# Optimization experiments

Hardware: AMD Instinct MI355X
Metric: run time of the kernel (lower is better)

The kernel has to match this reference:

```python
import jax, jax.numpy as jnp
import numpy as np

N = 3072          # n_vertices
D = 512           # embedding_size (hardcoded in module)
ALPHA = 0.2       # LeakyReLU slope
AVG_DEG = 32
NEG_INF = -9e15
N_ITERS = 10
TRIPLET_MARGIN = 400.0


def setup_inputs() -> dict:
    key = jax.random.key(0)
    ks = jax.random.split(key, 14)
    s = 0.05  # weight init scale
    emb = jax.random.normal(ks[0], (N, D), dtype=jnp.float32) * 0.1
    # symmetric 0/1 adjacency, no self loops, density ~ AVG_DEG/N
    u = jax.random.uniform(ks[1], (N, N))
    A = jnp.triu((u < (AVG_DEG / N)).astype(jnp.float32), 1)
    adj = A + A.T
    rn = lambda k, shp: jax.random.normal(k, shp, dtype=jnp.float32) * s
    return {
        "embeddings": emb,
        "adj": adj,
        "W_n": rn(ks[2], (D, D)), "a_src_n": rn(ks[3], (D,)), "a_dst_n": rn(ks[4], (D,)),
        "W_nn": rn(ks[5], (D, D)), "a_src_nn": rn(ks[6], (D,)), "a_dst_nn": rn(ks[7], (D,)),
        "W_u": rn(ks[8], (2 * D, D)), "b_u": jnp.zeros((D,), dtype=jnp.float32),
        "W_g": rn(ks[9], (D, D)), "a_src_g": rn(ks[10], (D,)), "a_dst_g": rn(ks[11], (D,)),
    }


def _gat_attention(h, adj, W, a_src, a_dst):
    # standard pyGAT layer: Wh = hW; e_ij = LeakyReLU(a_src.Wh_i + a_dst.Wh_j)
    Wh = h @ W                                   # [N, D]
    e = jax.nn.leaky_relu((Wh @ a_src)[:, None] + (Wh @ a_dst)[None, :], ALPHA)
    att = jax.nn.softmax(jnp.where(adj > 0, e, NEG_INF), axis=1)  # [N, N]
    return att, Wh


def reference(embeddings, adj, W_n, a_src_n, a_dst_n, W_nn, a_src_nn, a_dst_nn,
              W_u, b_u, W_g, a_src_g, a_dst_g):
    n = embeddings.shape[0]
    inv_adj = 1.0 - adj - jnp.eye(n, dtype=adj.dtype)  # non-neighbors, no self
    emb = embeddings
    for _ in range(N_ITERS):
        att_n, Wh_n = _gat_attention(emb, adj, W_n, a_src_n, a_dst_n)
        neigh = jax.nn.elu(att_n @ Wh_n)               # concat=True -> ELU
        att_nn, Wh_nn = _gat_attention(emb, inv_adj, W_nn, a_src_nn, a_dst_nn)
        non_neigh = jax.nn.elu(att_nn @ Wh_nn)
        cat = jnp.concatenate([neigh, non_neigh], axis=1)  # [N, 2D]
        emb = jax.nn.relu(emb + cat @ W_u + b_u)
    sq = jnp.sum(emb * emb, axis=1)
    d2 = sq[:, None] + sq[None, :] - 2.0 * (emb @ emb.T)
    dist = jnp.sqrt(jnp.maximum(d2, 1e-12))            # [N, N]
    embedding_loss = jnp.sum(dist * (-adj))
    triplet_loss = jnp.maximum(embedding_loss + TRIPLET_MARGIN, 0.0)
    # glimpse layer returns the attention matrix itself
    att_g, _ = _gat_attention(emb, adj, W_g, a_src_g, a_dst_g)
    confidence = jnp.max(att_g, axis=1)
    log_conf = jnp.mean(jnp.log(confidence + 1e-8) - jnp.log(1e-8))
    return jnp.stack([triplet_loss, embedding_loss, log_conf])
```

## Files before the change

### kernel.cpp

```cpp
#include <hip/hip_runtime.h>
#include <math.h>

#define N_V 3072
#define D_E 512
#define EDGE_CAP 128
constexpr float LRELU_ALPHA = 0.2f;
constexpr float NEG_INF_F = -9e15f;

typedef __attribute__((ext_vector_type(8))) short bf16x8;
typedef __attribute__((ext_vector_type(4))) float f32x4;
typedef __attribute__((ext_vector_type(4))) unsigned short ushort4v;
typedef __attribute__((ext_vector_type(2))) unsigned short ushort2v;

__device__ inline unsigned short f2bf(float f) {
    union { float f; unsigned int u; } x; x.f = f;
    unsigned int r = x.u + 0x7fffu + ((x.u >> 16) & 1u);
    return (unsigned short)(r >> 16);
}
__device__ inline float bf2f(unsigned short b) {
    union { unsigned int u; float f; } x; x.u = ((unsigned int)b) << 16;
    return x.f;
}

__device__ inline void xcd_swizzle(int& bx, int& by) {
    int gx = gridDim.x, nwg = gx * gridDim.y;
    int flat = by * gx + bx;
    int q = nwg >> 3;
    int swz = (flat & 7) * q + (flat >> 3);
    bx = swz % gx; by = swz / gx;
}

template<int EPI>
__global__ __launch_bounds__(256) void gemm_bf16(
    const unsigned short* __restrict__ A,
    const unsigned short* __restrict__ BT,
    int M, int N, int K,
    unsigned short* __restrict__ C0, int ldc0,
    unsigned short* __restrict__ C1,
    const float* __restrict__ addv,
    const float* __restrict__ bias,
    float* __restrict__ Cf)
{
    constexpr int BM = 128, BN = 64, BK = 64;
    __shared__ unsigned short As[BM * BK];
    __shared__ unsigned short Bs[BN * BK];
    const int tid  = threadIdx.x;
    int bxi = blockIdx.x, byi = blockIdx.y;
    xcd_swizzle(bxi, byi);
    const int bm   = byi * BM, bn = bxi * BN;
    const int lane = tid & 63, wid = tid >> 6;
    const int wr   = wid >> 1, wc = wid & 1;
    const int lr   = lane & 15, lk = lane >> 4;

    f32x4 acc[4][2];
    #pragma unroll
    for (int i = 0; i < 4; ++i)
        #pragma unroll
        for (int j = 0; j < 2; ++j)
            acc[i][j] = (f32x4)(0.f);

    auto asp = (__attribute__((address_space(3))) unsigned short*)As;
    auto bsp = (__attribute__((address_space(3))) unsigned short*)Bs;

    for (int k0 = 0; k0 < K; k0 += BK) {
        #pragma unroll
        for (int l = 0; l < 4; ++l) {
            int li = l * 256 + tid;
            int row = li >> 3, slot = li & 7;
            int gs = slot ^ (row & 7);
            __builtin_amdgcn_global_load_lds(
                (const __attribute__((address_space(1))) void*)(A + (size_t)(bm + row) * K + k0 + gs * 8),
                (__attribute__((address_space(3))) void*)(asp + li * 8), 16, 0, 0);
        }
        #pragma unroll
        for (int l = 0; l < 2; ++l) {
            int li = l * 256 + tid;
            int row = li >> 3, slot = li & 7;
            int gs = slot ^ (row & 7);
            __builtin_amdgcn_global_load_lds(
                (const __attribute__((address_space(1))) void*)(BT + (size_t)(bn + row) * K + k0 + gs * 8),
                (__attribute__((address_space(3))) void*)(bsp + li * 8), 16, 0, 0);
        }
        __syncthreads();

        #pragma unroll
        for (int ks = 0; ks < 2; ++ks) {
            bf16x8 af[4], bfr[2];
            #pragma unroll
            for (int fm = 0; fm < 4; ++fm) {
                int row = wr * 64 + fm * 16 + lr;
                int sl = (ks * 4 + lk) ^ (row & 7);
                af[fm] = *(const bf16x8*)(As + row * BK + sl * 8);
            }
            #pragma unroll
            for (int fn = 0; fn < 2; ++fn) {
                int col = wc * 32 + fn * 16 + lr;
                int sl = (ks * 4 + lk) ^ (col & 7);
                bfr[fn] = *(const bf16x8*)(Bs + col * BK + sl * 8);
            }
            #pragma unroll
            for (int fm = 0; fm < 4; ++fm)
                #pragma unroll
                for (int fn = 0; fn < 2; ++fn)
                    acc[fm][fn] = __builtin_amdgcn_mfma_f32_16x16x32_bf16(
                        af[fm], bfr[fn], acc[fm][fn], 0, 0, 0);
        }
        __syncthreads();
    }

    #pragma unroll
    for (int fm = 0; fm < 4; ++fm) {
        #pragma unroll
        for (int fn = 0; fn < 2; ++fn) {
            int row0 = bm + wr * 64 + fm * 16 + lk * 4;
            int col  = bn + wc * 32 + fn * 16 + lr;
            f32x4 v = acc[fm][fn];
            if (EPI == 2) {
                #pragma unroll
                for (int r = 0; r < 4; ++r) {
                    float x = v[r] + addv[(size_t)(row0 + r) * N + col] + bias[col];
                    x = x > 0.f ? x : 0.f;
                    Cf[(size_t)(row0 + r) * N + col] = x;
                    C0[(size_t)(row0 + r) * ldc0 + col] = f2bf(x);
                }
            } else {
                if (col < 512) {
                    #pragma unroll
                    for (int r = 0; r < 4; ++r)
                        C0[(size_t)(row0 + r) * ldc0 + col] = f2bf(v[r]);
                } else {
                    ushort4v p;
                    p.x = f2bf(v[0]); p.y = f2bf(v[1]);
                    p.z = f2bf(v[2]); p.w = f2bf(v[3]);
                    *(ushort4v*)(C1 + (size_t)(col - 512) * M + row0) = p;
                }
            }
        }
    }
}

__global__ __launch_bounds__(256) void gemm_nn64(
    const unsigned short* __restrict__ A,
    const unsigned short* __restrict__ BT,
    unsigned short* __restrict__ cat)
{
    constexpr int BM = 64, BN = 64, BK = 64, K = N_V;
    __shared__ unsigned short As[BM * BK];
    __shared__ unsigned short Bs[BN * BK];
    const int tid = threadIdx.x;
    int bxi = blockIdx.x, byi = blockIdx.y;
    xcd_swizzle(bxi, byi);
    const int bm = byi * BM, bn = bxi * BN;
    const int lane = tid & 63, wid = tid >> 6;
    const int wr = wid >> 1, wc = wid & 1;
    const int lr = lane & 15, lk = lane >> 4;

    f32x4 acc[2][2];
    #pragma unroll
    for (int i = 0; i < 2; ++i)
        #pragma unroll
        for (int j = 0; j < 2; ++j)
            acc[i][j] = (f32x4)(0.f);

    auto asp = (__attribute__((address_space(3))) unsigned short*)As;
    auto bsp = (__attribute__((address_space(3))) unsigned short*)Bs;

    for (int k0 = 0; k0 < K; k0 += BK) {
        #pragma unroll
        for (int l = 0; l < 2; ++l) {
            int li = l * 256 + tid;
            int row = li >> 3, slot = li & 7;
            int gs = slot ^ (row & 7);
            __builtin_amdgcn_global_load_lds(
                (const __attribute__((address_space(1))) void*)(A + (size_t)(bm + row) * K + k0 + gs * 8),
                (__attribute__((address_space(3))) void*)(asp + li * 8), 16, 0, 0);
        }
        #pragma unroll
        for (int l = 0; l < 2; ++l) {
            int li = l * 256 + tid;
            int row = li >> 3, slot = li & 7;
            int gs = slot ^ (row & 7);
            __builtin_amdgcn_global_load_lds(
                (const __attribute__((address_space(1))) void*)(BT + (size_t)(bn + row) * K + k0 + gs * 8),
                (__attribute__((address_space(3))) void*)(bsp + li * 8), 16, 0, 0);
        }
        __syncthreads();

        #pragma unroll
        for (int ks = 0; ks < 2; ++ks) {
            bf16x8 af[2], bfr[2];
            #pragma unroll
            for (int fm = 0; fm < 2; ++fm) {
                int row = wr * 32 + fm * 16 + lr;
                int sl = (ks * 4 + lk) ^ (row & 7);
                af[fm] = *(const bf16x8*)(As + row * BK + sl * 8);
            }
            #pragma unroll
            for (int fn = 0; fn < 2; ++fn) {
                int col = wc * 32 + fn * 16 + lr;
                int sl = (ks * 4 + lk) ^ (col & 7);
                bfr[fn] = *(const bf16x8*)(Bs + col * BK + sl * 8);
            }
            #pragma unroll
            for (int fm = 0; fm < 2; ++fm)
                #pragma unroll
                for (int fn = 0; fn < 2; ++fn)
                    acc[fm][fn] = __builtin_amdgcn_mfma_f32_16x16x32_bf16(
                        af[fm], bfr[fn], acc[fm][fn], 0, 0, 0);
        }
        __syncthreads();
    }

    #pragma unroll
    for (int fm = 0; fm < 2; ++fm) {
        #pragma unroll
        for (int fn = 0; fn < 2; ++fn) {
            int row0 = bm + wr * 32 + fm * 16 + lk * 4;
            int col  = bn + wc * 32 + fn * 16 + lr;
            #pragma unroll
            for (int r = 0; r < 4; ++r) {
                float x = acc[fm][fn][r];
                x = x > 0.f ? x : (expf(x) - 1.f);
                cat[(size_t)(row0 + r) * (2 * D_E) + D_E + col] = f2bf(x);
            }
        }
    }
}

__global__ __launch_bounds__(256) void convT_f32_bf16(
    const float* __restrict__ W, unsigned short* __restrict__ WT, int K, int Nw)
{
    int k = blockIdx.x * 256 + threadIdx.x;
    int n = blockIdx.y;
    if (k < K) WT[(size_t)n * K + k] = f2bf(W[(size_t)k * Nw + n]);
}

__global__ __launch_bounds__(256) void conv_bf16(
    const float* __restrict__ X, unsigned short* __restrict__ Y, int n)
{
    int i = blockIdx.x * 256 + threadIdx.x;
    if (i < n) Y[i] = f2bf(X[i]);
}

__global__ __launch_bounds__(256) void build_graph(
    const float* __restrict__ adj, int* __restrict__ edges,
    int* __restrict__ deg, unsigned int* __restrict__ bitmask)
{
    const int i = blockIdx.x, t = threadIdx.x;
    __shared__ int cnts[256];
    unsigned int word = 0;
    int c = 0;
    if (t < 96) {
        #pragma unroll
        for (int b = 0; b < 32; ++b) {
            int j = t * 32 + b;
            if (adj[(size_t)i * N_V + j] > 0.f) { word |= (1u << b); ++c; }
        }
    }
    cnts[t] = c;
    __syncthreads();
    for (int o = 1; o < 256; o <<= 1) {
        int add = (t >= o) ? cnts[t - o] : 0;
        __syncthreads();
        cnts[t] += add;
        __syncthreads();
    }
    int base = cnts[t] - c;
    if (t < 96) {
        int k = 0;
        #pragma unroll
        for (int b = 0; b < 32; ++b) {
            if ((word >> b) & 1u) {
                int pos = base + k;
                if (pos < EDGE_CAP) edges[(size_t)i * EDGE_CAP + pos] = t * 32 + b;
                ++k;
            }
        }
        bitmask[(size_t)i * 96 + t] = word;
    }
    if (t == 0) deg[i] = cnts[255] < EDGE_CAP ? cnts[255] : EDGE_CAP;
}

__global__ __launch_bounds__(256) void matvec6(
    const float* __restrict__ W_n, const float* __restrict__ W_nn,
    const float* __restrict__ W_g,
    const float* __restrict__ as_n, const float* __restrict__ ad_n,
    const float* __restrict__ as_nn, const float* __restrict__ ad_nn,
    const float* __restrict__ as_g, const float* __restrict__ ad_g,
    float* __restrict__ wv)
{
    const int wave = threadIdx.x >> 6, lane = threadIdx.x & 63;
    const int r = blockIdx.x * 4 + wave;
    float a0 = 0, a1 = 0, a2 = 0, a3 = 0, a4 = 0, a5 = 0;
    #pragma unroll
    for (int k = 0; k < 8; ++k) {
        int c = lane + k * 64;
        float wn = W_n[(size_t)r * D_E + c];
        float wm = W_nn[(size_t)r * D_E + c];
        float wg = W_g[(size_t)r * D_E + c];
        a0 = fmaf(wn, as_n[c], a0);  a1 = fmaf(wn, ad_n[c], a1);
        a2 = fmaf(wm, as_nn[c], a2); a3 = fmaf(wm, ad_nn[c], a3);
        a4 = fmaf(wg, as_g[c], a4);  a5 = fmaf(wg, ad_g[c], a5);
    }
    #pragma unroll
    for (int off = 32; off; off >>= 1) {
        a0 += __shfl_down(a0, off); a1 += __shfl_down(a1, off);
        a2 += __shfl_down(a2, off); a3 += __shfl_down(a3, off);
        a4 += __shfl_down(a4, off); a5 += __shfl_down(a5, off);
    }
    if (lane == 0) {
        wv[0 * D_E + r] = a0; wv[1 * D_E + r] = a1;
        wv[2 * D_E + r] = a2; wv[3 * D_E + r] = a3;
        wv[4 * D_E + r] = a4; wv[5 * D_E + r] = a5;
    }
}

template<int NV>
__global__ __launch_bounds__(256) void sd_dots(
    const unsigned short* __restrict__ emb, const float* __restrict__ wv,
    float* __restrict__ outs)
{
    const int wave = threadIdx.x >> 6, lane = threadIdx.x & 63;
    const int i = blockIdx.x * 4 + wave;
    float acc[NV];
    #pragma unroll
    for (int v = 0; v < NV; ++v) acc[v] = 0.f;
    #pragma unroll
    for (int k = 0; k < 8; ++k) {
        int c = lane + k * 64;
        float x = bf2f(emb[(size_t)i * D_E + c]);
        #pragma unroll
        for (int v = 0; v < NV; ++v) acc[v] = fmaf(x, wv[v * D_E + c], acc[v]);
    }
    #pragma unroll
    for (int off = 32; off; off >>= 1)
        #pragma unroll
        for (int v = 0; v < NV; ++v) acc[v] += __shfl_down(acc[v], off);
    if (lane == 0)
        #pragma unroll
        for (int v = 0; v < NV; ++v) outs[v * N_V + i] = acc[v];
}

__global__ __launch_bounds__(256) void nn_sm_gather(
    const unsigned int* __restrict__ bitmask,
    const int* __restrict__ edges, const int* __restrict__ deg,
    const float* __restrict__ sd,
    const unsigned short* __restrict__ Whn,
    unsigned short* __restrict__ att, unsigned short* __restrict__ cat)
{
    const int t = threadIdx.x;
    __shared__ float red[256];
    if (blockIdx.x < N_V) {
        const int i = blockIdx.x;
        const float* s = sd + 2 * N_V;
        const float* dvec = sd + 3 * N_V;
        __shared__ unsigned int mrow[96];
        if (t < 96) mrow[t] = bitmask[(size_t)i * 96 + t];
        __syncthreads();
        const float si = s[i];
        const float4* dv4 = (const float4*)dvec;
        float e[3][4];
        float mloc = -3.4e38f;
        #pragma unroll
        for (int l = 0; l < 3; ++l) {
            int jv = t + l * 256;
            float4 d = dv4[jv];
            int j0 = jv * 4;
            unsigned int w = mrow[j0 >> 5];
            #pragma unroll
            for (int c = 0; c < 4; ++c) {
                int j = j0 + c;
                bool keep = (((w >> (j & 31)) & 1u) == 0u) && (j != i);
                float x = si + ((const float*)&d)[c];
                x = x > 0.f ? x : LRELU_ALPHA * x;
                e[l][c] = keep ? x : NEG_INF_F;
                mloc = fmaxf(mloc, e[l][c]);
            }
        }
        red[t] = mloc; __syncthreads();
        for (int o = 128; o; o >>= 1) {
            if (t < o) red[t] = fmaxf(red[t], red[t + o]);
            __syncthreads();
        }
        float m = red[0]; __syncthreads();
        float zloc = 0.f;
        #pragma unroll
        for (int l = 0; l < 3; ++l)
            #pragma unroll
            for (int c = 0; c < 4; ++c) { e[l][c] = expf(e[l][c] - m); zloc += e[l][c]; }
        red[t] = zloc; __syncthreads();
        for (int o = 128; o; o >>= 1) {
            if (t < o) red[t] += red[t + o];
            __syncthreads();
        }
        const float zinv = 1.f / red[0];
        #pragma unroll
        for (int l = 0; l < 3; ++l) {
            int jv = t + l * 256;
            ushort4v p;
            p.x = f2bf(e[l][0] * zinv); p.y = f2bf(e[l][1] * zinv);
            p.z = f2bf(e[l][2] * zinv); p.w = f2bf(e[l][3] * zinv);
            *(ushort4v*)(att + (size_t)i * N_V + (size_t)jv * 4) = p;
        }
    } else {
        const int i = blockIdx.x - N_V;
        const float* s = sd;
        const float* dvec = sd + N_V;
        const int cnt = deg[i];
        __shared__ float p[EDGE_CAP];
        __shared__ int lst[EDGE_CAP];
        float ev = -3.4e38f;
        if (t < cnt) {
            int j = edges[(size_t)i * EDGE_CAP + t];
            lst[t] = j;
            float x = s[i] + dvec[j];
            x = x > 0.f ? x : LRELU_ALPHA * x;
            p[t] = x;
            ev = x;
        }
        red[t] = ev; __syncthreads();
        for (int o = 128; o; o >>= 1) {
            if (t < o) red[t] = fmaxf(red[t], red[t + o]);
            __syncthreads();
        }
        float m = red[0]; __syncthreads();
        float pe = 0.f;
        if (t < cnt) { pe = expf(p[t] - m); p[t] = pe; }
        red[t] = pe; __syncthreads();
        for (int o = 128; o; o >>= 1) {
            if (t < o) red[t] += red[t + o];
            __syncthreads();
        }
        const float zinv = 1.f / red[0];
        float a0 = 0.f, a1 = 0.f;
        for (int e = 0; e < cnt; ++e) {
            int j = lst[e];
            float w = p[e] * zinv;
            ushort2v h = *(const ushort2v*)(Whn + (size_t)j * D_E + t * 2);
            a0 = fmaf(w, bf2f(h.x), a0);
            a1 = fmaf(w, bf2f(h.y), a1);
        }
        a0 = a0 > 0.f ? a0 : (expf(a0) - 1.f);
        a1 = a1 > 0.f ? a1 : (expf(a1) - 1.f);
        ushort2v o2; o2.x = f2bf(a0); o2.y = f2bf(a1);
        *(ushort2v*)(cat + (size_t)i * (2 * D_E) + t * 2) = o2;
    }
}

__global__ __launch_bounds__(256) void colsum(
    const float* __restrict__ emb, float* __restrict__ musum)
{
    const int b = blockIdx.x, t = threadIdx.x;
    float s0 = 0.f, s1 = 0.f;
    for (int r = 0; r < 64; ++r) {
        const float* row = emb + (size_t)(b * 64 + r) * D_E;
        s0 += row[t];
        s1 += row[t + 256];
    }
    atomicAdd(&musum[t], s0);
    atomicAdd(&musum[t + 256], s1);
}

__global__ __launch_bounds__(256) void center_bf16(
    const float* __restrict__ emb, const float* __restrict__ musum,
    unsigned short* __restrict__ embc)
{
    int i = blockIdx.x * 256 + threadIdx.x;
    int c = i & (D_E - 1);
    embc[i] = f2bf(emb[i] - musum[c] * (1.f / N_V));
}

__global__ __launch_bounds__(256) void edge_loss_c(
    const int* __restrict__ edges, const int* __restrict__ deg,
    const unsigned short* __restrict__ embc, float* __restrict__ epart)
{
    __shared__ unsigned short rowi[D_E];
    __shared__ float gsum[16];
    const int i = blockIdx.x, t = threadIdx.x;
    if (t < 64) ((bf16x8*)rowi)[t] = ((const bf16x8*)(embc + (size_t)i * D_E))[t];
    __syncthreads();
    const int g = t >> 4, l = t & 15;
    const int cnt = deg[i];
    float sum = 0.f;
    for (int e = g; e < cnt; e += 16) {
        int j = edges[(size_t)i * EDGE_CAP + e];
        float d2 = 0.f;
        #pragma unroll
        for (int q = 0; q < 4; ++q) {
            int off = q * 128 + l * 8;
            bf16x8 a = *(const bf16x8*)(rowi + off);
            bf16x8 b = *(const bf16x8*)(embc + (size_t)j * D_E + off);
            #pragma unroll
            for (int k = 0; k < 8; ++k) {
                float df = bf2f(((unsigned short*)&a)[k]) -
                           bf2f(((unsigned short*)&b)[k]);
                d2 = fmaf(df, df, d2);
            }
        }
        #pragma unroll
        for (int msk = 1; msk < 16; msk <<= 1) d2 += __shfl_xor(d2, msk);
        if (l == 0) sum += sqrtf(fmaxf(d2, 1e-12f));
    }
    if (l == 0) gsum[g] = sum;
    __syncthreads();
    if (t == 0) {
        float tot = 0.f;
        #pragma unroll
        for (int k = 0; k < 16; ++k) tot += gsum[k];
        epart[i] = tot;
    }
}

__global__ __launch_bounds__(256) void conf_kernel(
    const unsigned int* __restrict__ bitmask, const float* __restrict__ s,
    const float* __restrict__ dvec, float* __restrict__ cpart)
{
    const int i = blockIdx.x, t = threadIdx.x;
    __shared__ unsigned int mrow[96];
    __shared__ float red[256];
    if (t < 96) mrow[t] = bitmask[(size_t)i * 96 + t];
    __syncthreads();
    const float si = s[i];
    const float4* dv4 = (const float4*)dvec;
    float e[3][4];
    float mloc = -3.4e38f;
    #pragma unroll
    for (int l = 0; l < 3; ++l) {
        int jv = t + l * 256;
        float4 d = dv4[jv];
        int j0 = jv * 4;
        unsigned int w = mrow[j0 >> 5];
        #pragma unroll
        for (int c = 0; c < 4; ++c) {
            int j = j0 + c;
            bool keep = ((w >> (j & 31)) & 1u) != 0u;
            float x = si + ((const float*)&d)[c];
            x = x > 0.f ? x : LRELU_ALPHA * x;
            e[l][c] = keep ? x : NEG_INF_F;
            mloc = fmaxf(mloc, e[l][c]);
        }
    }
    red[t] = mloc; __syncthreads();
    for (int o = 128; o; o >>= 1) {
        if (t < o) red[t] = fmaxf(red[t], red[t + o]);
        __syncthreads();
    }
    float m = red[0]; __syncthreads();
    float zloc = 0.f;
    #pragma unroll
    for (int l = 0; l < 3; ++l)
        #pragma unroll
        for (int c = 0; c < 4; ++c) zloc += expf(e[l][c] - m);
    red[t] = zloc; __syncthreads();
    for (int o = 128; o; o >>= 1) {
        if (t < o) red[t] += red[t + o];
        __syncthreads();
    }
    if (t == 0) cpart[i] = logf(1.f / red[0] + 1e-8f);
}

__global__ __launch_bounds__(256) void finalize2(
    const float* __restrict__ epart, const float* __restrict__ cpart,
    float* __restrict__ out)
{
    const int t = threadIdx.x;
    float e = 0.f, c = 0.f;
    #pragma unroll
    for (int k = 0; k < 12; ++k) {
        e += epart[t + k * 256];
        c += cpart[t + k * 256];
    }
    __shared__ float re[256], rc[256];
    re[t] = e; rc[t] = c;
    __syncthreads();
    for (int o = 128; o; o >>= 1) {
        if (t < o) { re[t] += re[t + o]; rc[t] += rc[t + o]; }
        __syncthreads();
    }
    if (t == 0) {
        float loss = -re[0];
        out[0] = fmaxf(loss + 400.f, 0.f);
        out[1] = loss;
        out[2] = rc[0] / (float)N_V - logf(1e-8f);
    }
}

extern "C" void kernel_launch(void* const* d_in, const int* in_sizes, int n_in,
                              void* d_out, int out_size, void* d_ws, size_t ws_size,
                              hipStream_t stream) {
    const float* emb_in   = (const float*)d_in[0];
    const float* adj      = (const float*)d_in[1];
    const float* W_n      = (const float*)d_in[2];
    const float* a_src_n  = (const float*)d_in[3];
    const float* a_dst_n  = (const float*)d_in[4];
    const float* W_nn     = (const float*)d_in[5];
    const float* a_src_nn = (const float*)d_in[6];
    const float* a_dst_nn = (const float*)d_in[7];
    const float* W_u      = (const float*)d_in[8];
    const float* b_u      = (const float*)d_in[9];
    const float* W_g      = (const float*)d_in[10];
    const float* a_src_g  = (const float*)d_in[11];
    const float* a_dst_g  = (const float*)d_in[12];
    float* out = (float*)d_out;

    char* p = (char*)d_ws;
    auto alloc = [&](size_t bytes) { char* r = p; p += (bytes + 255) & ~(size_t)255; return r; };

    unsigned short* att_nn  = (unsigned short*)alloc((size_t)N_V * N_V * 2);
    unsigned short* Whn     = (unsigned short*)alloc((size_t)N_V * D_E * 2);
    unsigned short* WhTnn   = (unsigned short*)alloc((size_t)D_E * N_V * 2);
    unsigned short* cat_bf  = (unsigned short*)alloc((size_t)N_V * 2 * D_E * 2);
    float*          embf[2] = { (float*)alloc((size_t)N_V * D_E * 4),
                                (float*)alloc((size_t)N_V * D_E * 4) };
    unsigned short* embb[2] = { (unsigned short*)alloc((size_t)N_V * D_E * 2),
                                (unsigned short*)alloc((size_t)N_V * D_E * 2) };
    unsigned short* embc    = (unsigned short*)alloc((size_t)N_V * D_E * 2);
    unsigned short* W2T     = (unsigned short*)alloc((size_t)(2 * D_E) * D_E * 2);
    unsigned short* WuT     = (unsigned short*)alloc((size_t)D_E * (2 * D_E) * 2);
    float*          wv      = (float*)alloc(6 * D_E * 4);
    float*          sd      = (float*)alloc(4 * N_V * 4);
    float*          sdg     = (float*)alloc(2 * N_V * 4);
    float*          musum   = (float*)alloc(D_E * 4);
    float*          epart   = (float*)alloc(N_V * 4);
    float*          cpart   = (float*)alloc(N_V * 4);
    int*            edges   = (int*)alloc((size_t)N_V * EDGE_CAP * 4);
    int*            deg     = (int*)alloc(N_V * 4);
    unsigned int*   bitmask = (unsigned int*)alloc((size_t)N_V * 96 * 4);

    dim3 blk(256);

    convT_f32_bf16<<<dim3(2, D_E), blk, 0, stream>>>(W_n, W2T, D_E, D_E);
    convT_f32_bf16<<<dim3(2, D_E), blk, 0, stream>>>(W_nn, W2T + (size_t)D_E * D_E, D_E, D_E);
    convT_f32_bf16<<<dim3(4, D_E), blk, 0, stream>>>(W_u, WuT, 2 * D_E, D_E);
    conv_bf16<<<(N_V * D_E) / 256, blk, 0, stream>>>(emb_in, embb[0], N_V * D_E);
    hipMemcpyAsync(embf[0], emb_in, (size_t)N_V * D_E * 4, hipMemcpyDeviceToDevice, stream);
    hipMemsetAsync(musum, 0, D_E * sizeof(float), stream);
    build_graph<<<N_V, blk, 0, stream>>>(adj, edges, deg, bitmask);
    matvec6<<<D_E / 4, blk, 0, stream>>>(W_n, W_nn, W_g, a_src_n, a_dst_n,
                                         a_src_nn, a_dst_nn, a_src_g, a_dst_g, wv);

    dim3 gW2(16, N_V / 128);
    dim3 gG(8, N_V / 128);
    dim3 gNN(D_E / 64, N_V / 64);

    int cur = 0;
    for (int it = 0; it < 10; ++it) {
        int nxt = cur ^ 1;
        sd_dots<4><<<N_V / 4, blk, 0, stream>>>(embb[cur], wv, sd);
        gemm_bf16<4><<<gW2, blk, 0, stream>>>(embb[cur], W2T, N_V, 2 * D_E, D_E,
                                              Whn, D_E, WhTnn, nullptr, nullptr, nullptr);
        nn_sm_gather<<<2 * N_V, blk, 0, stream>>>(bitmask, edges, deg, sd,
                                                  Whn, att_nn, cat_bf);
        gemm_nn64<<<gNN, blk, 0, stream>>>(att_nn, WhTnn, cat_bf);
        gemm_bf16<2><<<gG, blk, 0, stream>>>(cat_bf, WuT, N_V, D_E, 2 * D_E,
                                             embb[nxt], D_E, nullptr, embf[cur], b_u, embf[nxt]);
        cur = nxt;
    }

    colsum<<<N_V / 64, blk, 0, stream>>>(embf[cur], musum);
    center_bf16<<<(N_V * D_E) / 256, blk, 0, stream>>>(embf[cur], musum, embc);
    edge_loss_c<<<N_V, blk, 0, stream>>>(edges, deg, embc, epart);
    sd_dots<2><<<N_V / 4, blk, 0, stream>>>(embb[cur], wv + 4 * D_E, sdg);
    conf_kernel<<<N_V, blk, 0, stream>>>(bitmask, sdg, sdg + N_V, cpart);

    finalize2<<<1, blk, 0, stream>>>(epart, cpart, out);
}
```

Baseline: 884.6 us.

## Fuse attention score dot products into projection GEMM and stage transposed stores via LDS

Removes the per-iteration sd_dots kernel by appending the precomputed W·a vectors as extra bf16 columns of the projection weight, so the GEMM grid gains one column tile that writes the six score vectors into sd. The transposed WhTnn output is now staged through shared memory and written with wide coalesced stores instead of scattered 4-element stores. The scores now come from bf16 weights rather than fp32, which costs some accuracy, and the extra column tile is mostly padding work.

```diff
diff --git a/kernel.cpp b/kernel.cpp
--- a/kernel.cpp
+++ b/kernel.cpp
@@ -42,8 +42,8 @@
     float* __restrict__ Cf)
 {
     constexpr int BM = 128, BN = 64, BK = 64;
-    __shared__ unsigned short As[BM * BK];
-    __shared__ unsigned short Bs[BN * BK];
+    __shared__ unsigned short As[BM * BK + BN * BK];
+    unsigned short* Bs = As + BM * BK;
     const int tid  = threadIdx.x;
     int bxi = blockIdx.x, byi = blockIdx.y;
     xcd_swizzle(bxi, byi);
@@ -108,14 +108,14 @@
         __syncthreads();
     }
 
-    #pragma unroll
-    for (int fm = 0; fm < 4; ++fm) {
-        #pragma unroll
-        for (int fn = 0; fn < 2; ++fn) {
-            int row0 = bm + wr * 64 + fm * 16 + lk * 4;
-            int col  = bn + wc * 32 + fn * 16 + lr;
-            f32x4 v = acc[fm][fn];
-            if (EPI == 2) {
+    if (EPI == 2) {
+        #pragma unroll
+        for (int fm = 0; fm < 4; ++fm) {
+            #pragma unroll
+            for (int fn = 0; fn < 2; ++fn) {
+                int row0 = bm + wr * 64 + fm * 16 + lk * 4;
+                int col  = bn + wc * 32 + fn * 16 + lr;
+                f32x4 v = acc[fm][fn];
                 #pragma unroll
                 for (int r = 0; r < 4; ++r) {
                     float x = v[r] + addv[(size_t)(row0 + r) * N + col] + bias[col];
@@ -123,16 +123,55 @@
                     Cf[(size_t)(row0 + r) * N + col] = x;
                     C0[(size_t)(row0 + r) * ldc0 + col] = f2bf(x);
                 }
-            } else {
-                if (col < 512) {
+            }
+        }
+    } else {
+        if (bn < 512) {
+            #pragma unroll
+            for (int fm = 0; fm < 4; ++fm) {
+                #pragma unroll
+                for (int fn = 0; fn < 2; ++fn) {
+                    int row0 = bm + wr * 64 + fm * 16 + lk * 4;
+                    int col  = bn + wc * 32 + fn * 16 + lr;
                     #pragma unroll
                     for (int r = 0; r < 4; ++r)
-                        C0[(size_t)(row0 + r) * ldc0 + col] = f2bf(v[r]);
-                } else {
-                    ushort4v p;
-                    p.x = f2bf(v[0]); p.y = f2bf(v[1]);
-                    p.z = f2bf(v[2]); p.w = f2bf(v[3]);
-                    *(ushort4v*)(C1 + (size_t)(col - 512) * M + row0) = p;
+                        C0[(size_t)(row0 + r) * ldc0 + col] = f2bf(acc[fm][fn][r]);
+                }
+            }
+        } else if (bn < 1024) {
+            constexpr int TS = 136;
+            unsigned short* Ts = As;
+            #pragma unroll
+            for (int fm = 0; fm < 4; ++fm) {
+                #pragma unroll
+                for (int fn = 0; fn < 2; ++fn) {
+                    int rloc = wr * 64 + fm * 16 + lk * 4;
+                    int lc   = wc * 32 + fn * 16 + lr;
+                    ushort4v pk;
+                    pk.x = f2bf(acc[fm][fn][0]); pk.y = f2bf(acc[fm][fn][1]);
+                    pk.z = f2bf(acc[fm][fn][2]); pk.w = f2bf(acc[fm][fn][3]);
+                    *(ushort4v*)(Ts + lc * TS + rloc) = pk;
+                }
+            }
+            __syncthreads();
+            for (int idx = tid; idx < 64 * 16; idx += 256) {
+                int c = idx >> 4, seg = idx & 15;
+                bf16x8 pk = *(const bf16x8*)(Ts + c * TS + seg * 8);
+                *(bf16x8*)(C1 + (size_t)(bn - 512 + c) * M + bm + seg * 8) = pk;
+            }
+        } else {
+            #pragma unroll
+            for (int fm = 0; fm < 4; ++fm) {
+                #pragma unroll
+                for (int fn = 0; fn < 2; ++fn) {
+                    int row0 = bm + wr * 64 + fm * 16 + lk * 4;
+                    int col  = bn + wc * 32 + fn * 16 + lr;
+                    if (col >= 1024 && col < 1030) {
+                        int v = col - 1024;
+                        #pragma unroll
+                        for (int r = 0; r < 4; ++r)
+                            Cf[(size_t)v * N_V + row0 + r] = acc[fm][fn][r];
+                    }
                 }
             }
         }
@@ -240,6 +279,14 @@
 {
     int i = blockIdx.x * 256 + threadIdx.x;
     if (i < n) Y[i] = f2bf(X[i]);
+}
+
+__global__ __launch_bounds__(256) void conv_wv_rows(
+    const float* __restrict__ wv, unsigned short* __restrict__ W2Tx)
+{
+    int k = threadIdx.x + (blockIdx.x & 1) * 256;
+    int v = blockIdx.x >> 1;
+    W2Tx[(size_t)(1024 + v) * D_E + k] = f2bf(wv[v * D_E + k]);
 }
 
 __global__ __launch_bounds__(256) void build_graph(
@@ -615,10 +662,10 @@
     unsigned short* embb[2] = { (unsigned short*)alloc((size_t)N_V * D_E * 2),
                                 (unsigned short*)alloc((size_t)N_V * D_E * 2) };
     unsigned short* embc    = (unsigned short*)alloc((size_t)N_V * D_E * 2);
-    unsigned short* W2T     = (unsigned short*)alloc((size_t)(2 * D_E) * D_E * 2);
+    unsigned short* W2Tx    = (unsigned short*)alloc((size_t)1088 * D_E * 2);
     unsigned short* WuT     = (unsigned short*)alloc((size_t)D_E * (2 * D_E) * 2);
     float*          wv      = (float*)alloc(6 * D_E * 4);
-    float*          sd      = (float*)alloc(4 * N_V * 4);
+    float*          sd      = (float*)alloc(6 * N_V * 4);
     float*          sdg     = (float*)alloc(2 * N_V * 4);
     float*          musum   = (float*)alloc(D_E * 4);
     float*          epart   = (float*)alloc(N_V * 4);
@@ -629,8 +676,9 @@
 
     dim3 blk(256);
 
-    convT_f32_bf16<<<dim3(2, D_E), blk, 0, stream>>>(W_n, W2T, D_E, D_E);
-    convT_f32_bf16<<<dim3(2, D_E), blk, 0, stream>>>(W_nn, W2T + (size_t)D_E * D_E, D_E, D_E);
+    hipMemsetAsync(W2Tx, 0, (size_t)1088 * D_E * 2, stream);
+    convT_f32_bf16<<<dim3(2, D_E), blk, 0, stream>>>(W_n, W2Tx, D_E, D_E);
+    convT_f32_bf16<<<dim3(2, D_E), blk, 0, stream>>>(W_nn, W2Tx + (size_t)D_E * D_E, D_E, D_E);
     convT_f32_bf16<<<dim3(4, D_E), blk, 0, stream>>>(W_u, WuT, 2 * D_E, D_E);
     conv_bf16<<<(N_V * D_E) / 256, blk, 0, stream>>>(emb_in, embb[0], N_V * D_E);
     hipMemcpyAsync(embf[0], emb_in, (size_t)N_V * D_E * 4, hipMemcpyDeviceToDevice, stream);
@@ -638,17 +686,17 @@
     build_graph<<<N_V, blk, 0, stream>>>(adj, edges, deg, bitmask);
     matvec6<<<D_E / 4, blk, 0, stream>>>(W_n, W_nn, W_g, a_src_n, a_dst_n,
                                          a_src_nn, a_dst_nn, a_src_g, a_dst_g, wv);
-
-    dim3 gW2(16, N_V / 128);
+    conv_wv_rows<<<12, blk, 0, stream>>>(wv, W2Tx);
+
+    dim3 gW2(17, N_V / 128);
     dim3 gG(8, N_V / 128);
     dim3 gNN(D_E / 64, N_V / 64);
 
     int cur = 0;
     for (int it = 0; it < 10; ++it) {
         int nxt = cur ^ 1;
-        sd_dots<4><<<N_V / 4, blk, 0, stream>>>(embb[cur], wv, sd);
-        gemm_bf16<4><<<gW2, blk, 0, stream>>>(embb[cur], W2T, N_V, 2 * D_E, D_E,
-                                              Whn, D_E, WhTnn, nullptr, nullptr, nullptr);
+        gemm_bf16<5><<<gW2, blk, 0, stream>>>(embb[cur], W2Tx, N_V, 1088, D_E,
+                                              Whn, D_E, WhTnn, nullptr, nullptr, sd);
         nn_sm_gather<<<2 * N_V, blk, 0, stream>>>(bitmask, edges, deg, sd,
                                                   Whn, att_nn, cat_bf);
         gemm_nn64<<<gNN, blk, 0, stream>>>(att_nn, WhTnn, cat_bf);
```

Result: faster. 853.8 us (-3.5%).
